# Performance work log

Hardware: AMD Instinct MI355X
Metric: run time of the kernel (lower is better)

Reference implementation:

```python
import jax, jax.numpy as jnp
import numpy as np

N = 50000      # nodes
E = 800000     # edges
IN = 128       # in_channels
C = 32         # hidden_channels per head
H = 8          # heads
NC = 2         # num_classes
EPS = 1e-5     # batchnorm eps
SLOPE = 0.2    # leaky relu negative slope


def setup_inputs() -> dict:
    key = jax.random.key(0)
    ks = jax.random.split(key, 16)
    d = {}
    d["x"] = jax.random.normal(ks[0], (N, IN), dtype=jnp.float32)
    d["edge_index"] = jax.random.randint(ks[1], (2, E), 0, N, dtype=jnp.int64)
    # layer 0: IN -> H*C (concat)
    s0 = 1.0 / np.sqrt(IN)
    d["Wl0"] = jax.random.normal(ks[2], (IN, H * C), dtype=jnp.float32) * s0
    d["Wr0"] = jax.random.normal(ks[3], (IN, H * C), dtype=jnp.float32) * s0
    d["att0"] = jax.random.normal(ks[4], (H, C), dtype=jnp.float32) * (1.0 / np.sqrt(C))
    d["b0"] = jnp.zeros((H * C,), dtype=jnp.float32)
    d["g0"] = jnp.ones((H * C,), dtype=jnp.float32)
    d["be0"] = jnp.zeros((H * C,), dtype=jnp.float32)
    d["m0"] = jax.random.normal(ks[5], (H * C,), dtype=jnp.float32) * 0.1
    d["v0"] = jax.random.uniform(ks[6], (H * C,), dtype=jnp.float32, minval=0.5, maxval=1.5)
    # layer 1: H*C -> C (mean over heads, concat=False)
    s1 = 1.0 / np.sqrt(H * C)
    d["Wl1"] = jax.random.normal(ks[7], (H * C, H * C), dtype=jnp.float32) * s1
    d["Wr1"] = jax.random.normal(ks[8], (H * C, H * C), dtype=jnp.float32) * s1
    d["att1"] = jax.random.normal(ks[9], (H, C), dtype=jnp.float32) * (1.0 / np.sqrt(C))
    d["b1"] = jnp.zeros((C,), dtype=jnp.float32)
    d["g1"] = jnp.ones((C,), dtype=jnp.float32)
    d["be1"] = jnp.zeros((C,), dtype=jnp.float32)
    d["m1"] = jax.random.normal(ks[10], (C,), dtype=jnp.float32) * 0.1
    d["v1"] = jax.random.uniform(ks[11], (C,), dtype=jnp.float32, minval=0.5, maxval=1.5)
    # classifier C -> NC
    d["Wc"] = jax.random.normal(ks[12], (C, NC), dtype=jnp.float32) * (1.0 / np.sqrt(C))
    d["bc"] = jnp.zeros((NC,), dtype=jnp.float32)
    return d


def _gatv2_layer(x, src, dst, Wl, Wr, att, b, concat, num_nodes):
    # GATv2Conv (PyG semantics): x_l = source proj, x_r = target proj,
    # e_ij = att . LeakyReLU(x_l[j] + x_r[i]); softmax over incoming edges of i;
    # out_i = sum_j alpha_ij * x_l[j]. Self-loops are added (PyG default).
    nH, nC = att.shape
    xl = (x @ Wl).reshape(num_nodes, nH, nC)
    xr = (x @ Wr).reshape(num_nodes, nH, nC)
    e = xl[src] + xr[dst]                              # [E', H, C]
    e = jnp.where(e > 0, e, SLOPE * e)
    logits = jnp.einsum('ehc,hc->eh', e, att)          # [E', H]
    m = jax.ops.segment_max(logits, dst, num_segments=num_nodes)   # [N, H]
    ex = jnp.exp(logits - m[dst])
    denom = jax.ops.segment_sum(ex, dst, num_segments=num_nodes)   # [N, H]
    alpha = ex / denom[dst]                            # [E', H]
    msg = alpha[:, :, None] * xl[src]                  # [E', H, C]
    out = jax.ops.segment_sum(msg, dst, num_segments=num_nodes)    # [N, H, C]
    if concat:
        return out.reshape(num_nodes, nH * nC) + b
    return out.mean(axis=1) + b


def _bn(x, g, be, m, v):
    return (x - m) * jax.lax.rsqrt(v + EPS) * g + be


def reference(x, edge_index, Wl0, Wr0, att0, b0, g0, be0, m0, v0,
              Wl1, Wr1, att1, b1, g1, be1, m1, v1, Wc, bc):
    num_nodes = x.shape[0]
    loop = jnp.arange(num_nodes, dtype=edge_index.dtype)
    src = jnp.concatenate([edge_index[0], loop])
    dst = jnp.concatenate([edge_index[1], loop])
    h = _gatv2_layer(x, src, dst, Wl0, Wr0, att0, b0, True, num_nodes)
    h = _bn(h, g0, be0, m0, v0)
    h = jax.nn.elu(h)   # eval mode: dropout is identity
    h = _gatv2_layer(h, src, dst, Wl1, Wr1, att1, b1, False, num_nodes)
    h = _bn(h, g1, be1, m1, v1)
    return h @ Wc + bc
```

## Files before the change

### kernel.cpp

```cpp
#include <hip/hip_runtime.h>
#include <math.h>

#define N_NODES 50000
#define M_PAD   50048
#define E_EDGES 800000
#define IN_CH   128
#define C_CH    32
#define H_HEADS 8
#define HC      256
#define BN_EPS  1e-5f
#define SLOPE   0.2f
#define LOG2E   1.44269504f

#define SCAN_CHUNK 512
#define SCAN_B     ((N_NODES + SCAN_CHUNK - 1) / SCAN_CHUNK)

typedef _Float16 f16x8 __attribute__((ext_vector_type(8)));
typedef _Float16 f16x4 __attribute__((ext_vector_type(4)));
typedef _Float16 f16x2 __attribute__((ext_vector_type(2)));
typedef float    f32x4 __attribute__((ext_vector_type(4)));

#if __has_builtin(__builtin_amdgcn_exp2f)
#define EXP2F(x) __builtin_amdgcn_exp2f(x)
#else
#define EXP2F(x) exp2f(x)
#endif


__global__ void k_init_deg(int* deg, int n) {
    int i = blockIdx.x * blockDim.x + threadIdx.x;
    if (i < n) deg[i] = 1;
}

__global__ void k_hist(const int* __restrict__ dst, int* deg, int e) {
    int i = blockIdx.x * blockDim.x + threadIdx.x;
    if (i < e) atomicAdd(&deg[dst[i]], 1);
}

__global__ __launch_bounds__(256) void k_scan_local(
        const int* __restrict__ deg, int* __restrict__ row_ptr,
        int* __restrict__ partials, int n) {
    __shared__ int sm[256];
    int t = threadIdx.x;
    int base = blockIdx.x * SCAN_CHUNK;
    int i0 = base + 2 * t, i1 = i0 + 1;
    int a = (i0 < n) ? deg[i0] : 0;
    int b = (i1 < n) ? deg[i1] : 0;
    int s = a + b;
    sm[t] = s;
    __syncthreads();
    #pragma unroll
    for (int off = 1; off < 256; off <<= 1) {
        int u = (t >= off) ? sm[t - off] : 0;
        __syncthreads();
        sm[t] += u;
        __syncthreads();
    }
    int excl = sm[t] - s;
    if (i0 < n) row_ptr[i0] = excl;
    if (i1 < n) row_ptr[i1] = excl + a;
    if (t == 255) partials[blockIdx.x] = sm[255];
}

__global__ __launch_bounds__(128) void k_scan_part(
        int* __restrict__ partials, int* __restrict__ row_ptr_n) {
    __shared__ int sm[128];
    int t = threadIdx.x;
    int v = (t < SCAN_B) ? partials[t] : 0;
    sm[t] = v;
    __syncthreads();
    #pragma unroll
    for (int off = 1; off < 128; off <<= 1) {
        int u = (t >= off) ? sm[t - off] : 0;
        __syncthreads();
        sm[t] += u;
        __syncthreads();
    }
    if (t < SCAN_B) partials[t] = sm[t] - v;
    if (t == 127) *row_ptr_n = sm[127];
}

__global__ void k_scan_add(int* __restrict__ row_ptr, int* __restrict__ cursor,
                           const int* __restrict__ partials, int n) {
    int i = blockIdx.x * blockDim.x + threadIdx.x;
    if (i < n) {
        int v = row_ptr[i] + partials[i / SCAN_CHUNK];
        row_ptr[i] = v;
        cursor[i] = v;
    }
}

__global__ void k_fill(const int* __restrict__ src, const int* __restrict__ dst,
                       int* cursor, int* csr_src, int e, int n) {
    int i = blockIdx.x * blockDim.x + threadIdx.x;
    if (i < e) {
        int d = dst[i];
        int p = atomicAdd(&cursor[d], 1);
        csr_src[p] = src[i] << 9;
    } else if (i < e + n) {
        int v = i - e;
        int p = atomicAdd(&cursor[v], 1);
        csr_src[p] = v << 9;
    }
}


__global__ void k_split_w4(const float* __restrict__ Wl0, const float* __restrict__ Wr0,
                           const float* __restrict__ Wl1, const float* __restrict__ Wr1,
                           _Float16* __restrict__ W0lt, _Float16* __restrict__ W0rt,
                           _Float16* __restrict__ W1lt, _Float16* __restrict__ W1rt) {
    int t = blockIdx.x * blockDim.x + threadIdx.x;
    const float* W; _Float16* O; int K, rel;
    if (t < 32768)       { W = Wl0; O = W0lt; K = 128; rel = t; }
    else if (t < 65536)  { W = Wr0; O = W0rt; K = 128; rel = t - 32768; }
    else if (t < 131072) { W = Wl1; O = W1lt; K = 256; rel = t - 65536; }
    else if (t < 196608) { W = Wr1; O = W1rt; K = 256; rel = t - 131072; }
    else return;
    int n = rel / K, k = rel - n * K;
    O[rel] = (_Float16)W[(size_t)k * 256 + n];
}


#define BK  32
#define LDA 40

__device__ __forceinline__ f16x8 cvt_h8(float4 a, float4 b) {
    f16x8 v = { (_Float16)a.x, (_Float16)a.y, (_Float16)a.z, (_Float16)a.w,
                (_Float16)b.x, (_Float16)b.y, (_Float16)b.z, (_Float16)b.w };
    return v;
}

__global__ __launch_bounds__(512) void k_gemm_mfma(
        const _Float16* __restrict__ A16, const float* __restrict__ A32,
        const _Float16* __restrict__ W0t, const _Float16* __restrict__ W1t,
        _Float16* __restrict__ C0, _Float16* __restrict__ C1, int K) {
    __shared__ _Float16 As [128 * LDA];
    __shared__ _Float16 Bs0[128 * LDA];
    __shared__ _Float16 Bs1[128 * LDA];
    int t = threadIdx.x;
    int lane = t & 63, wv = t >> 6;
    int quad = lane >> 4, r16 = lane & 15;
    size_t mBase = (size_t)blockIdx.x * 128;
    size_t nBase = (size_t)blockIdx.y * 128;
    int sr = t >> 2;
    int sc = (t & 3) * 8;
    f32x4 acc0[8] = {}, acc1[8] = {};
    for (int k0 = 0; k0 < K; k0 += BK) {
        if (A32) {
            size_t r0 = mBase + sr;
            float4 a0 = {0.f, 0.f, 0.f, 0.f}, a1 = a0;
            if (r0 < N_NODES) {
                const float* g = A32 + r0 * K + k0 + sc;
                a0 = ((const float4*)g)[0];
                a1 = ((const float4*)g)[1];
            }
            *(f16x8*)&As[sr * LDA + sc] = cvt_h8(a0, a1);
        } else {
            *(f16x8*)&As[sr * LDA + sc] =
                *(const f16x8*)(A16 + (size_t)(mBase + sr) * K + k0 + sc);
        }
        *(f16x8*)&Bs0[sr * LDA + sc] = *(const f16x8*)(W0t + (size_t)(nBase + sr) * K + k0 + sc);
        *(f16x8*)&Bs1[sr * LDA + sc] = *(const f16x8*)(W1t + (size_t)(nBase + sr) * K + k0 + sc);
        __syncthreads();
        f16x8 av = *(f16x8*)&As[(wv * 16 + r16) * LDA + quad * 8];
        #pragma unroll
        for (int ni = 0; ni < 8; ++ni) {
            f16x8 bv0 = *(f16x8*)&Bs0[(ni * 16 + r16) * LDA + quad * 8];
            f16x8 bv1 = *(f16x8*)&Bs1[(ni * 16 + r16) * LDA + quad * 8];
            acc0[ni] = __builtin_amdgcn_mfma_f32_16x16x32_f16(av, bv0, acc0[ni], 0, 0, 0);
            acc1[ni] = __builtin_amdgcn_mfma_f32_16x16x32_f16(av, bv1, acc1[ni], 0, 0, 0);
        }
        __syncthreads();
    }
    #pragma unroll
    for (int r = 0; r < 4; ++r) {
        size_t row = mBase + wv * 16 + quad * 4 + r;
        _Float16* cp0 = C0 + row * 256 + nBase + r16;
        _Float16* cp1 = C1 + row * 256 + nBase + r16;
        #pragma unroll
        for (int ni = 0; ni < 8; ++ni) {
            cp0[ni * 16] = (_Float16)acc0[ni][r];
            cp1[ni * 16] = (_Float16)acc1[ni][r];
        }
    }
}


__device__ __forceinline__ float qreduce8(float p) {
#if __has_builtin(__builtin_amdgcn_mov_dpp)
    p += __builtin_bit_cast(float, __builtin_amdgcn_mov_dpp(
             __builtin_bit_cast(int, p), 0xB1, 0xF, 0xF, true));
    p += __builtin_bit_cast(float, __builtin_amdgcn_mov_dpp(
             __builtin_bit_cast(int, p), 0x4E, 0xF, 0xF, true));
#else
    p += __shfl_xor(p, 1);
    p += __shfl_xor(p, 2);
#endif
    p += __shfl_xor(p, 4);
    return p;
}

__device__ __forceinline__ float edge_w16(f16x4 h, f16x4 xr, f16x4 att) {
    f16x4 e = h + xr;
    f16x4 es = e * (_Float16)SLOPE;
    f16x4 l = __builtin_elementwise_max(e, es);
#if __has_builtin(__builtin_amdgcn_fdot2)
    f16x2 l01 = __builtin_shufflevector(l, l, 0, 1);
    f16x2 l23 = __builtin_shufflevector(l, l, 2, 3);
    f16x2 a01 = __builtin_shufflevector(att, att, 0, 1);
    f16x2 a23 = __builtin_shufflevector(att, att, 2, 3);
    float p = __builtin_amdgcn_fdot2(l01, a01, 0.f, false);
    p = __builtin_amdgcn_fdot2(l23, a23, p, false);
#else
    float p = (float)l[0] * (float)att[0];
    p = fmaf((float)l[1], (float)att[1], p);
    p = fmaf((float)l[2], (float)att[2], p);
    p = fmaf((float)l[3], (float)att[3], p);
#endif
    return EXP2F(qreduce8(p));
}

__device__ __forceinline__ float4 edge_accum(
        const char* __restrict__ xlb, f16x4 xr_h, f16x4 att_h,
        const int* __restrict__ csr_src, int beg, int end) {
    float4 acc = {0.f, 0.f, 0.f, 0.f};
    float S = 0.f;
    int j = beg;
    for (; j + 4 <= end; j += 4) {
        int o0 = csr_src[j];
        int o1 = csr_src[j + 1];
        int o2 = csr_src[j + 2];
        int o3 = csr_src[j + 3];
        f16x4 h0 = *(const f16x4*)(xlb + o0);
        f16x4 h1 = *(const f16x4*)(xlb + o1);
        f16x4 h2 = *(const f16x4*)(xlb + o2);
        f16x4 h3 = *(const f16x4*)(xlb + o3);
        float w0 = edge_w16(h0, xr_h, att_h);
        float w1 = edge_w16(h1, xr_h, att_h);
        float w2 = edge_w16(h2, xr_h, att_h);
        float w3 = edge_w16(h3, xr_h, att_h);
        S += (w0 + w1) + (w2 + w3);
        acc.x = fmaf((float)h0[0], w0, acc.x); acc.y = fmaf((float)h0[1], w0, acc.y);
        acc.z = fmaf((float)h0[2], w0, acc.z); acc.w = fmaf((float)h0[3], w0, acc.w);
        acc.x = fmaf((float)h1[0], w1, acc.x); acc.y = fmaf((float)h1[1], w1, acc.y);
        acc.z = fmaf((float)h1[2], w1, acc.z); acc.w = fmaf((float)h1[3], w1, acc.w);
        acc.x = fmaf((float)h2[0], w2, acc.x); acc.y = fmaf((float)h2[1], w2, acc.y);
        acc.z = fmaf((float)h2[2], w2, acc.z); acc.w = fmaf((float)h2[3], w2, acc.w);
        acc.x = fmaf((float)h3[0], w3, acc.x); acc.y = fmaf((float)h3[1], w3, acc.y);
        acc.z = fmaf((float)h3[2], w3, acc.z); acc.w = fmaf((float)h3[3], w3, acc.w);
    }
    for (; j < end; ++j) {
        int o = csr_src[j];
        f16x4 hv = *(const f16x4*)(xlb + o);
        float w = edge_w16(hv, xr_h, att_h);
        S += w;
        acc.x = fmaf((float)hv[0], w, acc.x); acc.y = fmaf((float)hv[1], w, acc.y);
        acc.z = fmaf((float)hv[2], w, acc.z); acc.w = fmaf((float)hv[3], w, acc.w);
    }
    float inv = 1.f / S;
    acc.x *= inv; acc.y *= inv; acc.z *= inv; acc.w *= inv;
    return acc;
}

__global__ __launch_bounds__(256) void k_edge0(
        const _Float16* __restrict__ xl, const _Float16* __restrict__ xr,
        const float* __restrict__ att,
        const int* __restrict__ row_ptr, const int* __restrict__ csr_src,
        const float* __restrict__ b0, const float* __restrict__ g0,
        const float* __restrict__ be0, const float* __restrict__ m0,
        const float* __restrict__ v0,
        _Float16* __restrict__ h0) {
    int lane = threadIdx.x & 63;
    int i = __builtin_amdgcn_readfirstlane(blockIdx.x * 4 + (threadIdx.x >> 6));
    const char* xlb = (const char*)xl + lane * 8;
    f16x4 xr_h = ((const f16x4*)xr)[(size_t)i * 64 + lane];
    float4 af = ((const float4*)att)[lane];
    f16x4 att_h = { (_Float16)(af.x * LOG2E), (_Float16)(af.y * LOG2E),
                    (_Float16)(af.z * LOG2E), (_Float16)(af.w * LOG2E) };
    int beg = row_ptr[i], end = row_ptr[i + 1];
    float4 r = edge_accum(xlb, xr_h, att_h, csr_src, beg, end);
    float4 bb = ((const float4*)b0)[lane];
    float4 gg = ((const float4*)g0)[lane];
    float4 ee = ((const float4*)be0)[lane];
    float4 mm = ((const float4*)m0)[lane];
    float4 vv = ((const float4*)v0)[lane];
    float4 o;
    o.x = (r.x + bb.x - mm.x) * rsqrtf(vv.x + BN_EPS) * gg.x + ee.x;
    o.y = (r.y + bb.y - mm.y) * rsqrtf(vv.y + BN_EPS) * gg.y + ee.y;
    o.z = (r.z + bb.z - mm.z) * rsqrtf(vv.z + BN_EPS) * gg.z + ee.z;
    o.w = (r.w + bb.w - mm.w) * rsqrtf(vv.w + BN_EPS) * gg.w + ee.w;
    o.x = o.x > 0.f ? o.x : expm1f(o.x);
    o.y = o.y > 0.f ? o.y : expm1f(o.y);
    o.z = o.z > 0.f ? o.z : expm1f(o.z);
    o.w = o.w > 0.f ? o.w : expm1f(o.w);
    f16x4 hh = { (_Float16)o.x, (_Float16)o.y, (_Float16)o.z, (_Float16)o.w };
    ((f16x4*)h0)[(size_t)i * 64 + lane] = hh;
}

__global__ __launch_bounds__(256) void k_edge1(
        const _Float16* __restrict__ xl, const _Float16* __restrict__ xr,
        const float* __restrict__ att,
        const int* __restrict__ row_ptr, const int* __restrict__ csr_src,
        const float* __restrict__ b1, const float* __restrict__ g1,
        const float* __restrict__ be1, const float* __restrict__ m1,
        const float* __restrict__ v1,
        const float* __restrict__ Wc, const float* __restrict__ bc,
        float* __restrict__ out) {
    int lane = threadIdx.x & 63;
    int q = lane & 7;
    int i = __builtin_amdgcn_readfirstlane(blockIdx.x * 4 + (threadIdx.x >> 6));
    const char* xlb = (const char*)xl + lane * 8;
    f16x4 xr_h = ((const f16x4*)xr)[(size_t)i * 64 + lane];
    float4 af = ((const float4*)att)[lane];
    f16x4 att_h = { (_Float16)(af.x * LOG2E), (_Float16)(af.y * LOG2E),
                    (_Float16)(af.z * LOG2E), (_Float16)(af.w * LOG2E) };
    int beg = row_ptr[i], end = row_ptr[i + 1];
    float4 r = edge_accum(xlb, xr_h, att_h, csr_src, beg, end);
    #pragma unroll
    for (int mask = 8; mask <= 32; mask <<= 1) {
        r.x += __shfl_xor(r.x, mask);
        r.y += __shfl_xor(r.y, mask);
        r.z += __shfl_xor(r.z, mask);
        r.w += __shfl_xor(r.w, mask);
    }
    float4 bb = ((const float4*)b1)[q];
    float4 gg = ((const float4*)g1)[q];
    float4 ee = ((const float4*)be1)[q];
    float4 mm = ((const float4*)m1)[q];
    float4 vv = ((const float4*)v1)[q];
    r.x = (r.x * 0.125f + bb.x - mm.x) * rsqrtf(vv.x + BN_EPS) * gg.x + ee.x;
    r.y = (r.y * 0.125f + bb.y - mm.y) * rsqrtf(vv.y + BN_EPS) * gg.y + ee.y;
    r.z = (r.z * 0.125f + bb.z - mm.z) * rsqrtf(vv.z + BN_EPS) * gg.z + ee.z;
    r.w = (r.w * 0.125f + bb.w - mm.w) * rsqrtf(vv.w + BN_EPS) * gg.w + ee.w;
    float4 wc0 = ((const float4*)Wc)[q * 2];
    float4 wc1 = ((const float4*)Wc)[q * 2 + 1];
    float o0 = r.x * wc0.x + r.y * wc0.z + r.z * wc1.x + r.w * wc1.z;
    float o1 = r.x * wc0.y + r.y * wc0.w + r.z * wc1.y + r.w * wc1.w;
    #pragma unroll
    for (int mask = 1; mask <= 4; mask <<= 1) {
        o0 += __shfl_xor(o0, mask);
        o1 += __shfl_xor(o1, mask);
    }
    if (lane == 0) {
        float2 ov = {o0 + bc[0], o1 + bc[1]};
        *(float2*)(out + (size_t)i * 2) = ov;
    }
}


extern "C" void kernel_launch(void* const* d_in, const int* in_sizes, int n_in,
                              void* d_out, int out_size, void* d_ws, size_t ws_size,
                              hipStream_t stream) {
    const float* x    = (const float*)d_in[0];
    const int*   ei   = (const int*)d_in[1];
    const float* Wl0  = (const float*)d_in[2];
    const float* Wr0  = (const float*)d_in[3];
    const float* att0 = (const float*)d_in[4];
    const float* b0   = (const float*)d_in[5];
    const float* g0   = (const float*)d_in[6];
    const float* be0  = (const float*)d_in[7];
    const float* m0   = (const float*)d_in[8];
    const float* v0   = (const float*)d_in[9];
    const float* Wl1  = (const float*)d_in[10];
    const float* Wr1  = (const float*)d_in[11];
    const float* att1 = (const float*)d_in[12];
    const float* b1   = (const float*)d_in[13];
    const float* g1   = (const float*)d_in[14];
    const float* be1  = (const float*)d_in[15];
    const float* m1   = (const float*)d_in[16];
    const float* v1   = (const float*)d_in[17];
    const float* Wc   = (const float*)d_in[18];
    const float* bc   = (const float*)d_in[19];
    float* out = (float*)d_out;

    const int N = N_NODES, E = E_EDGES;
    const int* srcp = ei;
    const int* dstp = ei + E;

    char* p = (char*)d_ws;
    _Float16* xlf = (_Float16*)p; p += (size_t)M_PAD * HC * 2;
    _Float16* xrf = (_Float16*)p; p += (size_t)M_PAD * HC * 2;
    _Float16* h0  = (_Float16*)p; p += (size_t)M_PAD * HC * 2;
    _Float16* W0lt = (_Float16*)p; p += (size_t)HC * IN_CH * 2;
    _Float16* W0rt = (_Float16*)p; p += (size_t)HC * IN_CH * 2;
    _Float16* W1lt = (_Float16*)p; p += (size_t)HC * HC * 2;
    _Float16* W1rt = (_Float16*)p; p += (size_t)HC * HC * 2;
    int* deg      = (int*)p;
    int* row_ptr  = deg + N;
    int* cursor   = row_ptr + (N + 1);
    int* partials = cursor + N;
    int* csr_src  = partials + ((SCAN_B + 3) & ~3);

    k_init_deg<<<(N + 255) / 256, 256, 0, stream>>>(deg, N);
    k_hist<<<(E + 255) / 256, 256, 0, stream>>>(dstp, deg, E);
    k_scan_local<<<SCAN_B, 256, 0, stream>>>(deg, row_ptr, partials, N);
    k_scan_part<<<1, 128, 0, stream>>>(partials, row_ptr + N);
    k_scan_add<<<(N + 255) / 256, 256, 0, stream>>>(row_ptr, cursor, partials, N);
    k_fill<<<(E + N + 255) / 256, 256, 0, stream>>>(srcp, dstp, cursor, csr_src, E, N);

    k_split_w4<<<768, 256, 0, stream>>>(Wl0, Wr0, Wl1, Wr1, W0lt, W0rt, W1lt, W1rt);

    dim3 ggrid(M_PAD / 128, 2);
    k_gemm_mfma<<<ggrid, 512, 0, stream>>>(nullptr, x, W0lt, W0rt, xlf, xrf, IN_CH);
    k_edge0<<<N / 4, 256, 0, stream>>>(xlf, xrf, att0, row_ptr, csr_src,
                                       b0, g0, be0, m0, v0, h0);
    k_gemm_mfma<<<ggrid, 512, 0, stream>>>(h0, nullptr, W1lt, W1rt, xlf, xrf, HC);
    k_edge1<<<N / 4, 256, 0, stream>>>(xlf, xrf, att1, row_ptr, csr_src,
                                       b1, g1, be1, m1, v1, Wc, bc, out);
}
```

Before: 387.7 us.

## Stage GEMM epilogue through LDS, fuse deg init, branchless edge tail

```diff
diff --git a/kernel.cpp b/kernel.cpp
--- a/kernel.cpp
+++ b/kernel.cpp
@@ -26,11 +26,6 @@
 #define EXP2F(x) exp2f(x)
 #endif
 
-
-__global__ void k_init_deg(int* deg, int n) {
-    int i = blockIdx.x * blockDim.x + threadIdx.x;
-    if (i < n) deg[i] = 1;
-}
 
 __global__ void k_hist(const int* __restrict__ dst, int* deg, int e) {
     int i = blockIdx.x * blockDim.x + threadIdx.x;
@@ -108,14 +103,15 @@
 __global__ void k_split_w4(const float* __restrict__ Wl0, const float* __restrict__ Wr0,
                            const float* __restrict__ Wl1, const float* __restrict__ Wr1,
                            _Float16* __restrict__ W0lt, _Float16* __restrict__ W0rt,
-                           _Float16* __restrict__ W1lt, _Float16* __restrict__ W1rt) {
+                           _Float16* __restrict__ W1lt, _Float16* __restrict__ W1rt,
+                           int* __restrict__ deg) {
     int t = blockIdx.x * blockDim.x + threadIdx.x;
     const float* W; _Float16* O; int K, rel;
     if (t < 32768)       { W = Wl0; O = W0lt; K = 128; rel = t; }
     else if (t < 65536)  { W = Wr0; O = W0rt; K = 128; rel = t - 32768; }
     else if (t < 131072) { W = Wl1; O = W1lt; K = 256; rel = t - 65536; }
     else if (t < 196608) { W = Wr1; O = W1rt; K = 256; rel = t - 131072; }
-    else return;
+    else { int i = t - 196608; if (i < N_NODES) deg[i] = 1; return; }
     int n = rel / K, k = rel - n * K;
     O[rel] = (_Float16)W[(size_t)k * 256 + n];
 }
@@ -123,6 +119,7 @@
 
 #define BK  32
 #define LDA 40
+#define CP  136
 
 __device__ __forceinline__ f16x8 cvt_h8(float4 a, float4 b) {
     f16x8 v = { (_Float16)a.x, (_Float16)a.y, (_Float16)a.z, (_Float16)a.w,
@@ -134,9 +131,10 @@
         const _Float16* __restrict__ A16, const float* __restrict__ A32,
         const _Float16* __restrict__ W0t, const _Float16* __restrict__ W1t,
         _Float16* __restrict__ C0, _Float16* __restrict__ C1, int K) {
-    __shared__ _Float16 As [128 * LDA];
-    __shared__ _Float16 Bs0[128 * LDA];
-    __shared__ _Float16 Bs1[128 * LDA];
+    __shared__ _Float16 smem[128 * CP];
+    _Float16* As  = smem;
+    _Float16* Bs0 = smem + 5120;
+    _Float16* Bs1 = smem + 10240;
     int t = threadIdx.x;
     int lane = t & 63, wv = t >> 6;
     int quad = lane >> 4, r16 = lane & 15;
@@ -172,31 +170,41 @@
         }
         __syncthreads();
     }
+    int erow = t >> 2;
+    int ec = (t & 3) * 8;
+    size_t obase = (mBase + erow) * 256 + nBase + ec;
     #pragma unroll
-    for (int r = 0; r < 4; ++r) {
-        size_t row = mBase + wv * 16 + quad * 4 + r;
-        _Float16* cp0 = C0 + row * 256 + nBase + r16;
-        _Float16* cp1 = C1 + row * 256 + nBase + r16;
+    for (int tab = 0; tab < 2; ++tab) {
+        __syncthreads();
         #pragma unroll
         for (int ni = 0; ni < 8; ++ni) {
-            cp0[ni * 16] = (_Float16)acc0[ni][r];
-            cp1[ni * 16] = (_Float16)acc1[ni][r];
+            #pragma unroll
+            for (int r = 0; r < 4; ++r) {
+                float v = tab ? acc1[ni][r] : acc0[ni][r];
+                smem[(wv * 16 + quad * 4 + r) * CP + ni * 16 + r16] = (_Float16)v;
+            }
         }
+        __syncthreads();
+        f16x8 v0 = *(const f16x8*)&smem[erow * CP + ec];
+        f16x8 v1 = *(const f16x8*)&smem[erow * CP + ec + 32];
+        f16x8 v2 = *(const f16x8*)&smem[erow * CP + ec + 64];
+        f16x8 v3 = *(const f16x8*)&smem[erow * CP + ec + 96];
+        _Float16* C = tab ? C1 : C0;
+        *(f16x8*)(C + obase)      = v0;
+        *(f16x8*)(C + obase + 32) = v1;
+        *(f16x8*)(C + obase + 64) = v2;
+        *(f16x8*)(C + obase + 96) = v3;
     }
 }
 
 
 __device__ __forceinline__ float qreduce8(float p) {
-#if __has_builtin(__builtin_amdgcn_mov_dpp)
     p += __builtin_bit_cast(float, __builtin_amdgcn_mov_dpp(
              __builtin_bit_cast(int, p), 0xB1, 0xF, 0xF, true));
     p += __builtin_bit_cast(float, __builtin_amdgcn_mov_dpp(
              __builtin_bit_cast(int, p), 0x4E, 0xF, 0xF, true));
-#else
-    p += __shfl_xor(p, 1);
-    p += __shfl_xor(p, 2);
-#endif
-    p += __shfl_xor(p, 4);
+    p += __builtin_bit_cast(float, __builtin_amdgcn_mov_dpp(
+             __builtin_bit_cast(int, p), 0x141, 0xF, 0xF, true));
     return p;
 }
 
@@ -249,13 +257,26 @@
         acc.x = fmaf((float)h3[0], w3, acc.x); acc.y = fmaf((float)h3[1], w3, acc.y);
         acc.z = fmaf((float)h3[2], w3, acc.z); acc.w = fmaf((float)h3[3], w3, acc.w);
     }
-    for (; j < end; ++j) {
-        int o = csr_src[j];
-        f16x4 hv = *(const f16x4*)(xlb + o);
-        float w = edge_w16(hv, xr_h, att_h);
-        S += w;
-        acc.x = fmaf((float)hv[0], w, acc.x); acc.y = fmaf((float)hv[1], w, acc.y);
-        acc.z = fmaf((float)hv[2], w, acc.z); acc.w = fmaf((float)hv[3], w, acc.w);
+    if (j < end) {
+        int rem = end - j;
+        int o0 = csr_src[j];
+        int o1 = csr_src[rem > 1 ? j + 1 : j];
+        int o2 = csr_src[rem > 2 ? j + 2 : j];
+        f16x4 h0 = *(const f16x4*)(xlb + o0);
+        f16x4 h1 = *(const f16x4*)(xlb + o1);
+        f16x4 h2 = *(const f16x4*)(xlb + o2);
+        float w0 = edge_w16(h0, xr_h, att_h);
+        float w1 = edge_w16(h1, xr_h, att_h);
+        float w2 = edge_w16(h2, xr_h, att_h);
+        if (rem < 2) w1 = 0.f;
+        if (rem < 3) w2 = 0.f;
+        S += w0 + w1 + w2;
+        acc.x = fmaf((float)h0[0], w0, acc.x); acc.y = fmaf((float)h0[1], w0, acc.y);
+        acc.z = fmaf((float)h0[2], w0, acc.z); acc.w = fmaf((float)h0[3], w0, acc.w);
+        acc.x = fmaf((float)h1[0], w1, acc.x); acc.y = fmaf((float)h1[1], w1, acc.y);
+        acc.z = fmaf((float)h1[2], w1, acc.z); acc.w = fmaf((float)h1[3], w1, acc.w);
+        acc.x = fmaf((float)h2[0], w2, acc.x); acc.y = fmaf((float)h2[1], w2, acc.y);
+        acc.z = fmaf((float)h2[2], w2, acc.z); acc.w = fmaf((float)h2[3], w2, acc.w);
     }
     float inv = 1.f / S;
     acc.x *= inv; acc.y *= inv; acc.z *= inv; acc.w *= inv;
@@ -391,14 +412,13 @@
     int* partials = cursor + N;
     int* csr_src  = partials + ((SCAN_B + 3) & ~3);
 
-    k_init_deg<<<(N + 255) / 256, 256, 0, stream>>>(deg, N);
+    k_split_w4<<<964, 256, 0, stream>>>(Wl0, Wr0, Wl1, Wr1,
+                                        W0lt, W0rt, W1lt, W1rt, deg);
     k_hist<<<(E + 255) / 256, 256, 0, stream>>>(dstp, deg, E);
     k_scan_local<<<SCAN_B, 256, 0, stream>>>(deg, row_ptr, partials, N);
     k_scan_part<<<1, 128, 0, stream>>>(partials, row_ptr + N);
     k_scan_add<<<(N + 255) / 256, 256, 0, stream>>>(row_ptr, cursor, partials, N);
     k_fill<<<(E + N + 255) / 256, 256, 0, stream>>>(srcp, dstp, cursor, csr_src, E, N);
-
-    k_split_w4<<<768, 256, 0, stream>>>(Wl0, Wr0, Wl1, Wr1, W0lt, W0rt, W1lt, W1rt);
 
     dim3 ggrid(M_PAD / 128, 2);
     k_gemm_mfma<<<ggrid, 512, 0, stream>>>(nullptr, x, W0lt, W0rt, xlf, xrf, IN_CH);
```

Result: faster. 378.6 us (-2.4%).
